# Performance work log

Hardware: AMD Instinct MI355X
Metric: run time of the kernel (lower is better)

The kernel has to match this reference:

```python
import jax, jax.numpy as jnp
import numpy as np

B, S, D, H, V = 4, 1024, 1024, 16, 1024
HD = D // H  # head_dim = 64
FF = 4 * D


def _layer_norm(x, g, b, eps=1e-5):
    mu = jnp.mean(x, axis=-1, keepdims=True)
    var = jnp.var(x, axis=-1, keepdims=True)
    return (x - mu) * jax.lax.rsqrt(var + eps) * g + b


def _pos_encoding(seq_len, d_model):
    # sinusoidal PE, matching PositionalEncoding buffer construction
    pos = jnp.arange(seq_len, dtype=jnp.float32)[:, None]
    div = jnp.exp(jnp.arange(0, d_model, 2, dtype=jnp.float32) * (-np.log(10000.0) / d_model))
    pe = jnp.zeros((seq_len, d_model), dtype=jnp.float32)
    pe = pe.at[:, 0::2].set(jnp.sin(pos * div))
    pe = pe.at[:, 1::2].set(jnp.cos(pos * div))
    return pe


def setup_inputs() -> dict:
    key = jax.random.key(0)
    ks = jax.random.split(key, 12)
    sc = 0.02
    return {
        "inputs": jax.random.randint(ks[0], (B, S), 0, V, dtype=jnp.int32),
        "targets": jax.random.randint(ks[1], (B, S), 0, V, dtype=jnp.int32),
        "wte": jax.random.normal(ks[2], (V, D), jnp.float32) * sc,
        "wq": jax.random.normal(ks[3], (D, D), jnp.float32) * sc,
        "bq": jnp.zeros((D,), jnp.float32),
        "wk": jax.random.normal(ks[4], (D, D), jnp.float32) * sc,
        "bk": jnp.zeros((D,), jnp.float32),
        "wv": jax.random.normal(ks[5], (D, D), jnp.float32) * sc,
        "bv": jnp.zeros((D,), jnp.float32),
        "wo": jax.random.normal(ks[6], (D, D), jnp.float32) * sc,
        "bo": jnp.zeros((D,), jnp.float32),
        "w1": jax.random.normal(ks[7], (D, FF), jnp.float32) * sc,
        "b1": jnp.zeros((FF,), jnp.float32),
        "w2": jax.random.normal(ks[8], (FF, D), jnp.float32) * sc,
        "b2": jnp.zeros((D,), jnp.float32),
        "ln1_g": jnp.ones((D,), jnp.float32),
        "ln1_b": jnp.zeros((D,), jnp.float32),
        "ln2_g": jnp.ones((D,), jnp.float32),
        "ln2_b": jnp.zeros((D,), jnp.float32),
    }


def reference(inputs, targets, wte, wq, bq, wk, bk, wv, bv, wo, bo,
              w1, b1, w2, b2, ln1_g, ln1_b, ln2_g, ln2_b):
    # embedding + positional encoding
    x = wte[inputs] + _pos_encoding(S, D)  # [B,S,D]

    # naive causal multi-head attention (dropout = identity in eval)
    q = (x @ wq + bq).reshape(B, S, H, HD)
    k = (x @ wk + bk).reshape(B, S, H, HD)
    v = (x @ wv + bv).reshape(B, S, H, HD)
    scores = jnp.einsum('bqhd,bkhd->bhqk', q, k) / np.sqrt(HD)  # [B,H,S,S]
    causal = jnp.tril(jnp.ones((S, S), dtype=bool))
    scores = jnp.where(causal, scores, -jnp.inf)
    attn = jax.nn.softmax(scores, axis=-1)
    ctx = jnp.einsum('bhqk,bkhd->bqhd', attn, v).reshape(B, S, D)
    att_out = ctx @ wo + bo

    # residual + LN1, FFN + GELU, residual + LN2
    adn = _layer_norm(x + att_out, ln1_g, ln1_b)
    h = jax.nn.gelu(adn @ w1 + b1, approximate=False) @ w2 + b2
    logits = _layer_norm(h + adn, ln2_g, ln2_b)

    # cross-entropy over d_model(=vocab) classes
    logits_flat = logits.reshape(B * S, D)
    tgt = targets.reshape(B * S)
    logp = jax.nn.log_softmax(logits_flat, axis=-1)
    loss = -jnp.mean(jnp.take_along_axis(logp, tgt[:, None], axis=-1))
    return logits_flat, loss
```

## Files before the change

### kernel.cpp

```cpp
#include <hip/hip_runtime.h>
#include <math.h>

#define BB 4
#define SS 1024
#define DD 1024
#define HH 16
#define HDIM 64
#define FF 4096
#define MM 4096

typedef short bf16x8 __attribute__((ext_vector_type(8)));
typedef short bf16x4 __attribute__((ext_vector_type(4)));
typedef float f32x4  __attribute__((ext_vector_type(4)));

static __device__ __forceinline__ short f2bf(float f){
  unsigned u = __float_as_uint(f);
  u += 0x7FFFu + ((u >> 16) & 1u);
  return (short)(u >> 16);
}
static __device__ __forceinline__ float b2f(short s){
  return __uint_as_float(((unsigned)(unsigned short)s) << 16);
}

static __device__ __forceinline__ float erf_fast(float x){
  float ax = fabsf(x);
  float t  = __builtin_amdgcn_rcpf(1.0f + 0.3275911f * ax);
  float p  = t * (0.254829592f + t * (-0.284496736f + t * (1.421413741f +
             t * (-1.453152027f + t * 1.061405429f))));
  float e  = 1.0f - p * __expf(-ax * ax);
  return copysignf(e, x);
}

static __device__ __forceinline__ void gl_lds16(const short* g, short* l){
  __builtin_amdgcn_global_load_lds((const __attribute__((address_space(1))) unsigned int*)g,
                                   (__attribute__((address_space(3))) unsigned int*)l,
                                   16, 0, 0);
}

#define MFMA_BF16 __builtin_amdgcn_mfma_f32_16x16x32_bf16

__global__ __launch_bounds__(256) void trans_all_kernel(
    const float* __restrict__ wq, const float* __restrict__ wk,
    const float* __restrict__ wv, const float* __restrict__ wo,
    const float* __restrict__ w1, const float* __restrict__ w2,
    short* __restrict__ wqkvt, short* __restrict__ wot,
    short* __restrict__ w1t,   short* __restrict__ w2t){
  __shared__ float t[32][33];
  int idx = blockIdx.x;
  const float* src; short* dst; int R, C, cx, ry;
  if (idx < 4096){
    int wsel = idx >> 10, tt = idx & 1023;
    cx = tt & 31; ry = tt >> 5; R = 1024; C = 1024;
    src = (wsel == 0) ? wq : (wsel == 1) ? wk : (wsel == 2) ? wv : wo;
    dst = (wsel == 3) ? wot : wqkvt + (size_t)wsel * 1024 * 1024;
  } else if (idx < 8192){
    int tt = idx - 4096; cx = tt & 127; ry = tt >> 7; R = 1024; C = 4096;
    src = w1; dst = w1t;
  } else {
    int tt = idx - 8192; cx = tt & 31; ry = tt >> 5; R = 4096; C = 1024;
    src = w2; dst = w2t;
  }
  int c0 = cx * 32, r0 = ry * 32;
  int tx = threadIdx.x, ty = threadIdx.y;
#pragma unroll
  for (int i = 0; i < 32; i += 8)
    t[ty + i][tx] = src[(size_t)(r0 + ty + i) * C + (c0 + tx)];
  __syncthreads();
#pragma unroll
  for (int i = 0; i < 32; i += 8)
    dst[(size_t)(c0 + ty + i) * R + (r0 + tx)] = f2bf(t[tx][ty + i]);
}

__global__ __launch_bounds__(256) void concat_bias_kernel(const float* __restrict__ a,
                                                          const float* __restrict__ b,
                                                          const float* __restrict__ c,
                                                          float* __restrict__ dst){
  int t = blockIdx.x * 256 + threadIdx.x;
  float v = (t < 1024) ? a[t] : (t < 2048 ? b[t - 1024] : c[t - 2048]);
  dst[t] = v;
}

__global__ __launch_bounds__(256) void embed_kernel(const int* __restrict__ inputs,
                                                    const float* __restrict__ wte,
                                                    short* __restrict__ xb){
  int idx4 = blockIdx.x * 256 + threadIdx.x;
  int row = idx4 >> 8;
  int d   = (idx4 & 255) * 4;
  int s   = row & (SS - 1);
  int tok = inputs[row];
  float4 w = *(const float4*)&wte[(size_t)tok * DD + d];
  const float cdiv = -9.210340371976184f / 512.0f;
  int i0 = d >> 1;
  float ang0 = (float)s * expf((float)i0 * cdiv);
  float ang1 = (float)s * expf((float)(i0 + 1) * cdiv);
  float x0 = w.x + sinf(ang0);
  float x1 = w.y + cosf(ang0);
  float x2 = w.z + sinf(ang1);
  float x3 = w.w + cosf(ang1);
  bf16x4 sb; sb[0]=f2bf(x0); sb[1]=f2bf(x1); sb[2]=f2bf(x2); sb[3]=f2bf(x3);
  *(bf16x4*)&xb[(size_t)row * DD + d] = sb;
}

template<int MODE, bool GELU, bool ADDBIAS>
__global__ __launch_bounds__(512, 2) void gemm256_kernel(const short* __restrict__ A,
    const short* __restrict__ Bt, const float* __restrict__ bias,
    short* __restrict__ o0, short* __restrict__ o1,
    short* __restrict__ o2, short* __restrict__ o3,
    short* __restrict__ qo, short* __restrict__ ko, short* __restrict__ vto,
    int M, int N, int K, int Kc){
  __shared__ __align__(16) short lds[8 * 8192];
  int tid = threadIdx.x;
  int lid = blockIdx.y * gridDim.x + blockIdx.x;
  int cpx = (gridDim.x * gridDim.y) >> 3;
  int swz = (lid & 7) * cpx + (lid >> 3);
  int n0 = (swz % gridDim.x) * 256;
  int m0 = (swz / gridDim.x) * 256;
  int bz = blockIdx.z;
  int kbeg = bz * Kc;
  int w = tid >> 6, lane = tid & 63, lr = lane & 15, lg = lane >> 4;
  int wm = w >> 2, wn = w & 3;
  f32x4 acc[8][4] = {};

  int sr = lane >> 3;
  int sg = (lane & 7) ^ sr;
  auto STAGE_HALF = [&](int buf, int typ, int half, int kt){
    const short* s0 = (typ ? Bt : A) + (size_t)kbeg + sg * 8;
    int rb = (typ ? n0 : m0) + half * 128 + w * 8 + sr;
#pragma unroll
    for (int j = 0; j < 2; j++)
      gl_lds16(s0 + (size_t)(rb + j * 64) * K + kt * 64,
               &lds[(((buf << 2) | (typ << 1) | half) << 13) + (j << 12) + (w << 9)]);
  };

  int nt = Kc >> 6;
  STAGE_HALF(0, 0, 0, 0); STAGE_HALF(0, 0, 1, 0);
  STAGE_HALF(0, 1, 0, 0); STAGE_HALF(0, 1, 1, 0);
  STAGE_HALF(1, 0, 0, 1); STAGE_HALF(1, 0, 1, 1);
  STAGE_HALF(1, 1, 0, 1); STAGE_HALF(1, 1, 1, 1);
  asm volatile("s_waitcnt vmcnt(8)" ::: "memory");
  __builtin_amdgcn_s_barrier();

  int lr64 = lr * 64;
  int ck0 = ((lg     ) ^ (lr & 7)) * 8;
  int ck1 = ((lg + 4 ) ^ (lr & 7)) * 8;
  int brow = (wn & 1) << 12;

  bf16x8 Alo[4][2], Ahi[4][2], Blo[2][2], Bhi[2][2];

#define ABASE(b) ((((b) << 2) | wm) << 13) + lr64
#define BBASE(b) ((((b) << 2) | 2 | (wn >> 1)) << 13) + brow + lr64
#define RD_ALO(b) { int ab_ = ABASE(b); _Pragma("unroll") for (int fi_ = 0; fi_ < 4; fi_++){ \
    Alo[fi_][0] = *(const bf16x8*)&lds[ab_ + fi_ * 1024 + ck0]; \
    Alo[fi_][1] = *(const bf16x8*)&lds[ab_ + fi_ * 1024 + ck1]; } }
#define RD_AHI(b) { int ab_ = ABASE(b); _Pragma("unroll") for (int fi_ = 0; fi_ < 4; fi_++){ \
    Ahi[fi_][0] = *(const bf16x8*)&lds[ab_ + (fi_ + 4) * 1024 + ck0]; \
    Ahi[fi_][1] = *(const bf16x8*)&lds[ab_ + (fi_ + 4) * 1024 + ck1]; } }
#define RD_BLO(b) { int bb_ = BBASE(b); _Pragma("unroll") for (int ni_ = 0; ni_ < 2; ni_++){ \
    Blo[ni_][0] = *(const bf16x8*)&lds[bb_ + ni_ * 1024 + ck0]; \
    Blo[ni_][1] = *(const bf16x8*)&lds[bb_ + ni_ * 1024 + ck1]; } }
#define RD_BHI(b) { int bb_ = BBASE(b); _Pragma("unroll") for (int ni_ = 0; ni_ < 2; ni_++){ \
    Bhi[ni_][0] = *(const bf16x8*)&lds[bb_ + (ni_ + 2) * 1024 + ck0]; \
    Bhi[ni_][1] = *(const bf16x8*)&lds[bb_ + (ni_ + 2) * 1024 + ck1]; } }
#define QUAD(MB, NB, AF, BF) \
    __builtin_amdgcn_s_setprio(1); \
    _Pragma("unroll") for (int mi_ = 0; mi_ < 4; mi_++) \
      _Pragma("unroll") for (int ni_ = 0; ni_ < 2; ni_++){ \
        acc[mi_ + MB][ni_ + NB] = MFMA_BF16(AF[mi_][0], BF[ni_][0], acc[mi_ + MB][ni_ + NB], 0, 0, 0); \
        acc[mi_ + MB][ni_ + NB] = MFMA_BF16(AF[mi_][1], BF[ni_][1], acc[mi_ + MB][ni_ + NB], 0, 0, 0); } \
    __builtin_amdgcn_s_setprio(0);

  RD_ALO(0); RD_BLO(0);

  for (int t = 0; t < nt; t++){
    int b = t & 1, bn = b ^ 1;
    RD_AHI(b);
    asm volatile("s_waitcnt lgkmcnt(8)" ::: "memory");
    __builtin_amdgcn_sched_barrier(0);
    QUAD(0, 0, Alo, Blo);
    __builtin_amdgcn_s_barrier();
    RD_BHI(b);
    if (t + 2 < nt){ STAGE_HALF(b, 0, 0, t + 2); STAGE_HALF(b, 0, 1, t + 2); }
    asm volatile("s_waitcnt lgkmcnt(4)" ::: "memory");
    __builtin_amdgcn_sched_barrier(0);
    QUAD(4, 0, Ahi, Blo);
    __builtin_amdgcn_s_barrier();
    if (t + 2 < nt) asm volatile("s_waitcnt vmcnt(4)" ::: "memory");
    else            asm volatile("s_waitcnt vmcnt(0)" ::: "memory");
    if (t + 2 < nt){ STAGE_HALF(b, 1, 0, t + 2); STAGE_HALF(b, 1, 1, t + 2); }
    asm volatile("s_waitcnt lgkmcnt(0)" ::: "memory");
    __builtin_amdgcn_sched_barrier(0);
    QUAD(4, 2, Ahi, Bhi);
    __builtin_amdgcn_s_barrier();
    QUAD(0, 2, Alo, Bhi);
    __builtin_amdgcn_sched_barrier(0);
    if (t + 1 < nt){ RD_ALO(bn); RD_BLO(bn); }
    __builtin_amdgcn_s_barrier();
  }
#undef QUAD
#undef RD_BHI
#undef RD_BLO
#undef RD_AHI
#undef RD_ALO
#undef BBASE
#undef ABASE

  short* slab = (MODE == 1) ? ((bz == 0) ? o0 : (bz == 1) ? o1 : (bz == 2) ? o2 : o3) : o0;
  bool addb = ADDBIAS && (MODE != 1 || bz == 0);
#pragma unroll
  for (int mi = 0; mi < 8; mi++){
#pragma unroll
    for (int ni = 0; ni < 4; ni++){
      int ng = n0 + wn * 64 + ni * 16 + lr;
      float bv = addb ? bias[ng] : 0.0f;
      int mg0 = m0 + wm * 128 + mi * 16 + 4 * lg;
      if (MODE == 2){
        int sel = n0 >> 10;
        if (sel == 2){
          int d = ng & 1023; int hh = d >> 6, nn = d & 63;
          int bI = mg0 >> 10, sI = mg0 & 1023;
          bf16x4 pk;
#pragma unroll
          for (int r = 0; r < 4; r++) pk[r] = f2bf(acc[mi][ni][r] + bv);
          *(bf16x4*)&vto[(((size_t)(bI * HH + hh)) * HDIM + nn) * SS + sI] = pk;
        } else {
          short* dst = (sel == 0) ? qo : ko;
          float qscl = (sel == 0) ? 0.125f : 1.0f;
#pragma unroll
          for (int r = 0; r < 4; r++)
            dst[(size_t)(mg0 + r) * DD + (ng & 1023)] = f2bf((acc[mi][ni][r] + bv) * qscl);
        }
      } else {
#pragma unroll
        for (int r = 0; r < 4; r++){
          float v = acc[mi][ni][r] + bv;
          if (GELU) v = 0.5f * v * (1.0f + erf_fast(v * 0.70710678118654752f));
          slab[(size_t)(mg0 + r) * N + ng] = f2bf(v);
        }
      }
    }
  }
}

__global__ __launch_bounds__(256) void attn_kernel(const short* __restrict__ qb,
                                                   const short* __restrict__ kb,
                                                   const short* __restrict__ vtb,
                                                   short* __restrict__ ctxb){
  __shared__ __align__(16) short k_lds[2][64 * 64];
  __shared__ __align__(16) short v_lds[2][64 * 64];
  __shared__ __align__(16) short p_lds[4][2][16 * 72];
  int qp = blockIdx.x, h = blockIdx.y, b = blockIdx.z;
  int Tlo = qp, Thi = 15 - qp;
  int tid = threadIdx.x, w = tid >> 6, lane = tid & 63, lr = lane & 15, lg = lane >> 4;

  const short* kp0 = kb  + (size_t)b * SS * DD + h * HDIM;
  const short* vt0 = vtb + (size_t)(b * HH + h) * HDIM * SS;

  bf16x8 qf0[2], qf1[2];
#pragma unroll
  for (int ti = 0; ti < 2; ti++){
    int T = ti ? Thi : Tlo;
    const short* qp_ = qb + ((size_t)(b * SS + T * 64 + w * 16 + lr) * DD + h * HDIM);
    qf0[ti] = *(const bf16x8*)&qp_[lg * 8];
    qf1[ti] = *(const bf16x8*)&qp_[32 + lg * 8];
  }

  bf16x8 ones;
#pragma unroll
  for (int j = 0; j < 8; j++) ones[j] = (short)0x3F80;

  float m[2][4], l[2][4];
  f32x4 acc[2][4] = {};
#pragma unroll
  for (int ti = 0; ti < 2; ti++)
#pragma unroll
    for (int r = 0; r < 4; r++){ m[ti][r] = -1e30f; l[ti][r] = 0.0f; }

  int srow8 = lane >> 3;
  int sjs   = (lane & 7) ^ srow8;
  auto STAGE = [&](int buf, int kt){
#pragma unroll
    for (int i = 0; i < 2; i++){
      int rb  = (w + 4 * i) * 8;
      int row = rb + srow8;
      gl_lds16(kp0 + (size_t)(kt * 64 + row) * DD + sjs * 8, &k_lds[buf][rb * 64]);
      gl_lds16(vt0 + (size_t)row * SS + kt * 64 + sjs * 8,   &v_lds[buf][rb * 64]);
    }
  };

  int cur = 0;
  STAGE(0, 0);
  asm volatile("s_waitcnt vmcnt(0)" ::: "memory");
  __syncthreads();

  bf16x8 pf0[2], pf1[2];
  for (int kt = 0; kt <= Thi; kt++){
    if (kt < Thi) STAGE(cur ^ 1, kt + 1);

    bf16x8 kf0[4], kf1[4];
#pragma unroll
    for (int sub = 0; sub < 4; sub++){
      int r = sub * 16 + lr;
      kf0[sub] = *(const bf16x8*)&k_lds[cur][r * 64 + ((lg     ^ (r & 7)) * 8)];
      kf1[sub] = *(const bf16x8*)&k_lds[cur][r * 64 + (((lg+4) ^ (r & 7)) * 8)];
    }

#pragma unroll
    for (int ti = 0; ti < 2; ti++){
      int T = ti ? Thi : Tlo;
      if (kt > T) continue;
      f32x4 sc4[4];
      __builtin_amdgcn_s_setprio(1);
#pragma unroll
      for (int sub = 0; sub < 4; sub++){
        f32x4 t = {};
        t = MFMA_BF16(qf0[ti], kf0[sub], t, 0, 0, 0);
        t = MFMA_BF16(qf1[ti], kf1[sub], t, 0, 0, 0);
        sc4[sub] = t;
      }
      __builtin_amdgcn_s_setprio(0);
      if (kt == T){
#pragma unroll
        for (int sub = 0; sub < 4; sub++)
#pragma unroll
          for (int r = 0; r < 4; r++)
            if (16 * sub + lr > 16 * w + 4 * lg + r) sc4[sub][r] = -1e30f;
      }

      float pm[4];
#pragma unroll
      for (int r = 0; r < 4; r++)
        pm[r] = fmaxf(fmaxf(sc4[0][r], sc4[1][r]), fmaxf(sc4[2][r], sc4[3][r]));
#pragma unroll
      for (int off = 1; off < 16; off <<= 1)
#pragma unroll
        for (int r = 0; r < 4; r++) pm[r] = fmaxf(pm[r], __shfl_xor(pm[r], off));

      float dmax = fmaxf(fmaxf(pm[0] - m[ti][0], pm[1] - m[ti][1]),
                         fmaxf(pm[2] - m[ti][2], pm[3] - m[ti][3]));
      if (!__all(dmax <= 8.0f)){
        float scl[4];
#pragma unroll
        for (int r = 0; r < 4; r++){
          float mn = fmaxf(m[ti][r], pm[r]);
          scl[r] = __expf(m[ti][r] - mn);
          m[ti][r] = mn;
          l[ti][r] *= scl[r];
        }
#pragma unroll
        for (int nb = 0; nb < 4; nb++)
#pragma unroll
          for (int r = 0; r < 4; r++) acc[ti][nb][r] *= scl[r];
      }

      short* pw = &p_lds[w][ti][0];
#pragma unroll
      for (int sub = 0; sub < 4; sub++)
#pragma unroll
        for (int r = 0; r < 4; r++)
          pw[(4 * lg + r) * 72 + sub * 16 + lr] = f2bf(__expf(sc4[sub][r] - m[ti][r]));
      pf0[ti] = *(const bf16x8*)&pw[lr * 72 + lg * 8];
      pf1[ti] = *(const bf16x8*)&pw[lr * 72 + 32 + lg * 8];
    }

    bf16x8 vf0[4], vf1[4];
#pragma unroll
    for (int nb = 0; nb < 4; nb++){
      int r = nb * 16 + lr;
      vf0[nb] = *(const bf16x8*)&v_lds[cur][r * 64 + ((lg     ^ (r & 7)) * 8)];
      vf1[nb] = *(const bf16x8*)&v_lds[cur][r * 64 + (((lg+4) ^ (r & 7)) * 8)];
    }

#pragma unroll
    for (int ti = 0; ti < 2; ti++){
      int T = ti ? Thi : Tlo;
      if (kt > T) continue;
      f32x4 rsum = {};
      __builtin_amdgcn_s_setprio(1);
      rsum = MFMA_BF16(pf0[ti], ones, rsum, 0, 0, 0);
      rsum = MFMA_BF16(pf1[ti], ones, rsum, 0, 0, 0);
#pragma unroll
      for (int nb = 0; nb < 4; nb++){
        acc[ti][nb] = MFMA_BF16(pf0[ti], vf0[nb], acc[ti][nb], 0, 0, 0);
        acc[ti][nb] = MFMA_BF16(pf1[ti], vf1[nb], acc[ti][nb], 0, 0, 0);
      }
      __builtin_amdgcn_s_setprio(0);
#pragma unroll
      for (int r = 0; r < 4; r++) l[ti][r] += rsum[r];
    }

    asm volatile("s_waitcnt vmcnt(0)" ::: "memory");
    __syncthreads();
    cur ^= 1;
  }

#pragma unroll
  for (int ti = 0; ti < 2; ti++){
    int T = ti ? Thi : Tlo;
#pragma unroll
    for (int r = 0; r < 4; r++){
      float inv = 1.0f / l[ti][r];
      int row = T * 64 + w * 16 + 4 * lg + r;
#pragma unroll
      for (int nb = 0; nb < 4; nb++)
        ctxb[(size_t)(b * SS + row) * DD + h * HDIM + nb * 16 + lr] = f2bf(acc[ti][nb][r] * inv);
    }
  }
}

template<int NPART, bool WF32, bool LOSS>
__global__ __launch_bounds__(256) void ln_kernel(const short* __restrict__ p0,
                                                 const short* __restrict__ p1,
                                                 const short* __restrict__ p2,
                                                 const short* __restrict__ p3,
                                                 const short* __restrict__ resb,
                                                 const float* __restrict__ g,
                                                 const float* __restrict__ be,
                                                 float* __restrict__ of,
                                                 short* __restrict__ ob,
                                                 const int* __restrict__ tgt,
                                                 float* __restrict__ lrow){
  int row = blockIdx.x, tid = threadIdx.x;
  size_t base = (size_t)row * DD + tid * 4;
  bf16x4 rv = *(const bf16x4*)&resb[base];
  float x0 = b2f(rv[0]), x1 = b2f(rv[1]), x2 = b2f(rv[2]), x3 = b2f(rv[3]);
  const short* ps[4] = {p0, p1, p2, p3};
#pragma unroll
  for (int p = 0; p < NPART; p++){
    bf16x4 pv = *(const bf16x4*)&ps[p][base];
    x0 += b2f(pv[0]); x1 += b2f(pv[1]); x2 += b2f(pv[2]); x3 += b2f(pv[3]);
  }
  float s = x0 + x1 + x2 + x3;
  float q = x0 * x0 + x1 * x1 + x2 * x2 + x3 * x3;
#pragma unroll
  for (int off = 32; off; off >>= 1){ s += __shfl_xor(s, off); q += __shfl_xor(q, off); }
  __shared__ float red[9];
  if ((tid & 63) == 0){ red[tid >> 6] = s; red[4 + (tid >> 6)] = q; }
  __syncthreads();
  s = red[0] + red[1] + red[2] + red[3];
  q = red[4] + red[5] + red[6] + red[7];
  float mean = s * (1.0f / DD);
  float var  = q * (1.0f / DD) - mean * mean;
  float rstd = rsqrtf(var + 1e-5f);
  float4 gv  = *(const float4*)&g[tid * 4];
  float4 bev = *(const float4*)&be[tid * 4];
  float y0 = (x0 - mean) * rstd * gv.x + bev.x;
  float y1 = (x1 - mean) * rstd * gv.y + bev.y;
  float y2 = (x2 - mean) * rstd * gv.z + bev.z;
  float y3 = (x3 - mean) * rstd * gv.w + bev.w;
  if (WF32){
    *(float4*)&of[base] = make_float4(y0, y1, y2, y3);
  } else {
    bf16x4 sb; sb[0]=f2bf(y0); sb[1]=f2bf(y1); sb[2]=f2bf(y2); sb[3]=f2bf(y3);
    *(bf16x4*)&ob[base] = sb;
  }
  if (LOSS){
    __syncthreads();
    float mx = fmaxf(fmaxf(y0, y1), fmaxf(y2, y3));
#pragma unroll
    for (int off = 32; off; off >>= 1) mx = fmaxf(mx, __shfl_xor(mx, off));
    if ((tid & 63) == 0) red[tid >> 6] = mx;
    int t = tgt[row];
    if (tid == (t >> 2))
      red[8] = ((t & 3) == 0) ? y0 : ((t & 3) == 1) ? y1 : ((t & 3) == 2) ? y2 : y3;
    __syncthreads();
    mx = fmaxf(fmaxf(red[0], red[1]), fmaxf(red[2], red[3]));
    float se = __expf(y0 - mx) + __expf(y1 - mx) + __expf(y2 - mx) + __expf(y3 - mx);
#pragma unroll
    for (int off = 32; off; off >>= 1) se += __shfl_xor(se, off);
    if ((tid & 63) == 0) red[4 + (tid >> 6)] = se;
    __syncthreads();
    if (tid == 0){
      float tot = red[4] + red[5] + red[6] + red[7];
      lrow[row] = mx + logf(tot) - red[8];
    }
  }
}

__global__ __launch_bounds__(256) void loss_reduce_kernel(const float* __restrict__ pr,
                                                          float* __restrict__ outp){
  int tid = threadIdx.x;
  float s = 0.0f;
  for (int i = tid; i < MM; i += 256) s += pr[i];
#pragma unroll
  for (int off = 32; off; off >>= 1) s += __shfl_xor(s, off);
  __shared__ float red[4];
  if ((tid & 63) == 0) red[tid >> 6] = s;
  __syncthreads();
  if (tid == 0) outp[0] = (red[0] + red[1] + red[2] + red[3]) * (1.0f / MM);
}

extern "C" void kernel_launch(void* const* d_in, const int* in_sizes, int n_in,
                              void* d_out, int out_size, void* d_ws, size_t ws_size,
                              hipStream_t stream){
  const int*   inputs  = (const int*)  d_in[0];
  const int*   targets = (const int*)  d_in[1];
  const float* wte     = (const float*)d_in[2];
  const float* wq      = (const float*)d_in[3];
  const float* bq      = (const float*)d_in[4];
  const float* wk      = (const float*)d_in[5];
  const float* bk      = (const float*)d_in[6];
  const float* wv      = (const float*)d_in[7];
  const float* bvv     = (const float*)d_in[8];
  const float* wo      = (const float*)d_in[9];
  const float* bo      = (const float*)d_in[10];
  const float* w1      = (const float*)d_in[11];
  const float* b1      = (const float*)d_in[12];
  const float* w2      = (const float*)d_in[13];
  const float* b2      = (const float*)d_in[14];
  const float* ln1g    = (const float*)d_in[15];
  const float* ln1b    = (const float*)d_in[16];
  const float* ln2g    = (const float*)d_in[17];
  const float* ln2b    = (const float*)d_in[18];
  float* out = (float*)d_out;

  char* ws = (char*)d_ws;
  const size_t MB = 1024 * 1024;
  short* wqkvt = (short*)(ws + 0 * MB);
  short* wot   = (short*)(ws + 6 * MB);
  short* w1t   = (short*)(ws + 8 * MB);
  short* w2t   = (short*)(ws + 16 * MB);
  short* xb    = (short*)(ws + 24 * MB);
  short* qbuf  = (short*)(ws + 32 * MB);
  short* kbuf  = (short*)(ws + 40 * MB);
  short* vtb   = (short*)(ws + 48 * MB);
  short* ctxb  = (short*)(ws + 56 * MB);
  short* pr0   = (short*)(ws + 64 * MB);
  short* pr1   = (short*)(ws + 72 * MB);
  short* pr2   = (short*)(ws + 80 * MB);
  short* pr3   = (short*)(ws + 88 * MB);
  short* adnb  = (short*)(ws + 96 * MB);
  short* h1b   = (short*)(ws + 32 * MB);
  short* hs0   = (short*)(ws + 64 * MB);
  short* hs1   = (short*)(ws + 72 * MB);
  short* hs2   = (short*)(ws + 80 * MB);
  short* hs3   = (short*)(ws + 88 * MB);
  float* lrow  = (float*)(ws + 104 * MB);
  float* bqkv  = (float*)(ws + 105 * MB);

  trans_all_kernel<<<12288, dim3(32, 8), 0, stream>>>(
      wq, wk, wv, wo, w1, w2, wqkvt, wot, w1t, w2t);
  concat_bias_kernel<<<12, 256, 0, stream>>>(bq, bk, bvv, bqkv);

  embed_kernel<<<4096, 256, 0, stream>>>(inputs, wte, xb);

  gemm256_kernel<2, false, true><<<dim3(12, 16), 512, 0, stream>>>(
      xb, wqkvt, bqkv, nullptr, nullptr, nullptr, nullptr,
      qbuf, kbuf, vtb, MM, 3 * DD, DD, DD);

  attn_kernel<<<dim3(8, 16, 4), 256, 0, stream>>>(qbuf, kbuf, vtb, ctxb);

  gemm256_kernel<1, false, true><<<dim3(4, 16, 4), 512, 0, stream>>>(
      ctxb, wot, bo, pr0, pr1, pr2, pr3,
      nullptr, nullptr, nullptr, MM, DD, DD, 256);

  ln_kernel<4, false, false><<<4096, 256, 0, stream>>>(
      pr0, pr1, pr2, pr3, xb, ln1g, ln1b, nullptr, adnb, nullptr, nullptr);

  gemm256_kernel<0, true, true><<<dim3(16, 16), 512, 0, stream>>>(
      adnb, w1t, b1, h1b, nullptr, nullptr, nullptr,
      nullptr, nullptr, nullptr, MM, FF, DD, DD);

  gemm256_kernel<1, false, true><<<dim3(4, 16, 4), 512, 0, stream>>>(
      h1b, w2t, b2, hs0, hs1, hs2, hs3,
      nullptr, nullptr, nullptr, MM, DD, FF, 1024);

  ln_kernel<4, true, true><<<4096, 256, 0, stream>>>(
      hs0, hs1, hs2, hs3, adnb, ln2g, ln2b, out, nullptr, targets, lrow);

  loss_reduce_kernel<<<1, 256, 0, stream>>>(lrow, out + (size_t)MM * DD);
}
```

Before: 219.2 us.

## Add 128x256-tile GEMM variant for output projection and FFN GEMMs

Introduces a new GEMM kernel that uses a 128x256 output tile instead of 256x256, with 8 waves laid out 2x4 and each wave computing 64x64. It double-buffers LDS, uses XOR-swizzled LDS reads, and applies a block-id swizzle for L2 locality. The output projection, FFN1 and FFN2 GEMMs switch to it with twice as many blocks, aiming for better CU occupancy and load balance on the 256-CU device. The cost is lower arithmetic intensity per block and more redundant B-tile loads.

```diff
diff --git a/kernel.cpp b/kernel.cpp
--- a/kernel.cpp
+++ b/kernel.cpp
@@ -241,6 +241,90 @@
   }
 }
 
+template<int MODE, bool GELU, bool ADDBIAS>
+__global__ __launch_bounds__(512) void gemmw_kernel(const short* __restrict__ A,
+    const short* __restrict__ Bt, const float* __restrict__ bias,
+    short* __restrict__ o0, short* __restrict__ o1,
+    short* __restrict__ o2, short* __restrict__ o3,
+    int M, int N, int K, int Kc){
+  __shared__ __align__(16) short lds[2][12288];
+  int tid = threadIdx.x;
+  int lid = blockIdx.y * gridDim.x + blockIdx.x;
+  int cpx = (gridDim.x * gridDim.y) >> 3;
+  int swz = (lid & 7) * cpx + (lid >> 3);
+  int n0 = (swz % gridDim.x) * 256;
+  int m0 = (swz / gridDim.x) * 128;
+  int bz = blockIdx.z;
+  int kbeg = bz * Kc;
+  int w = tid >> 6, lane = tid & 63, lr = lane & 15, lg = lane >> 4;
+  int wm = w >> 2, wn = w & 3;
+  f32x4 acc[4][4] = {};
+
+  int sr = lane >> 2;
+  int sg = (lane & 3) ^ ((lane >> 3) & 3);
+  const short* Arow = A  + (size_t)(m0 + w * 16 + sr) * K + kbeg + sg * 8;
+  const short* Brow = Bt + (size_t)(n0 + w * 16 + sr) * K + kbeg + sg * 8;
+
+  auto STAGE = [&](int buf, int kt){
+    int k0 = kt * 32;
+    gl_lds16(Arow + k0, &lds[buf][w * 512]);
+#pragma unroll
+    for (int j = 0; j < 2; j++)
+      gl_lds16(Brow + (size_t)(j * 128) * K + k0, &lds[buf][4096 + j * 4096 + w * 512]);
+  };
+
+  int nst = Kc >> 5;
+  STAGE(0, 0);
+  asm volatile("s_waitcnt vmcnt(0)" ::: "memory");
+  __builtin_amdgcn_s_barrier();
+
+  int cxor = ((lr >> 1) & 3) * 8;
+
+  for (int it = 0; it < nst; it++){
+    int cur = it & 1;
+    if (it + 1 < nst) STAGE(cur ^ 1, it + 1);
+
+    bf16x8 af[4], bfr[4];
+#pragma unroll
+    for (int mi = 0; mi < 4; mi++){
+      int row = wm * 64 + mi * 16 + lr;
+      af[mi] = *(const bf16x8*)&lds[cur][row * 32 + ((lg * 8) ^ cxor)];
+    }
+#pragma unroll
+    for (int ni = 0; ni < 4; ni++){
+      int row = wn * 64 + ni * 16 + lr;
+      bfr[ni] = *(const bf16x8*)&lds[cur][4096 + row * 32 + ((lg * 8) ^ cxor)];
+    }
+    __builtin_amdgcn_s_setprio(1);
+#pragma unroll
+    for (int mi = 0; mi < 4; mi++)
+#pragma unroll
+      for (int ni = 0; ni < 4; ni++)
+        acc[mi][ni] = MFMA_BF16(af[mi], bfr[ni], acc[mi][ni], 0, 0, 0);
+    __builtin_amdgcn_s_setprio(0);
+    asm volatile("s_waitcnt vmcnt(0) lgkmcnt(0)" ::: "memory");
+    __builtin_amdgcn_s_barrier();
+  }
+
+  short* slab = (MODE == 1) ? ((bz == 0) ? o0 : (bz == 1) ? o1 : (bz == 2) ? o2 : o3) : o0;
+  bool addb = ADDBIAS && (MODE != 1 || bz == 0);
+#pragma unroll
+  for (int mi = 0; mi < 4; mi++){
+#pragma unroll
+    for (int ni = 0; ni < 4; ni++){
+      int ng = n0 + wn * 64 + ni * 16 + lr;
+      float bv = addb ? bias[ng] : 0.0f;
+      int mg0 = m0 + wm * 64 + mi * 16 + 4 * lg;
+#pragma unroll
+      for (int r = 0; r < 4; r++){
+        float v = acc[mi][ni][r] + bv;
+        if (GELU) v = 0.5f * v * (1.0f + erf_fast(v * 0.70710678118654752f));
+        slab[(size_t)(mg0 + r) * N + ng] = f2bf(v);
+      }
+    }
+  }
+}
+
 __global__ __launch_bounds__(256) void attn_kernel(const short* __restrict__ qb,
                                                    const short* __restrict__ kb,
                                                    const short* __restrict__ vtb,
@@ -549,20 +633,17 @@
 
   attn_kernel<<<dim3(8, 16, 4), 256, 0, stream>>>(qbuf, kbuf, vtb, ctxb);
 
-  gemm256_kernel<1, false, true><<<dim3(4, 16, 4), 512, 0, stream>>>(
-      ctxb, wot, bo, pr0, pr1, pr2, pr3,
-      nullptr, nullptr, nullptr, MM, DD, DD, 256);
+  gemmw_kernel<1, false, true><<<dim3(4, 32, 4), 512, 0, stream>>>(
+      ctxb, wot, bo, pr0, pr1, pr2, pr3, MM, DD, DD, 256);
 
   ln_kernel<4, false, false><<<4096, 256, 0, stream>>>(
       pr0, pr1, pr2, pr3, xb, ln1g, ln1b, nullptr, adnb, nullptr, nullptr);
 
-  gemm256_kernel<0, true, true><<<dim3(16, 16), 512, 0, stream>>>(
-      adnb, w1t, b1, h1b, nullptr, nullptr, nullptr,
-      nullptr, nullptr, nullptr, MM, FF, DD, DD);
-
-  gemm256_kernel<1, false, true><<<dim3(4, 16, 4), 512, 0, stream>>>(
-      h1b, w2t, b2, hs0, hs1, hs2, hs3,
-      nullptr, nullptr, nullptr, MM, DD, FF, 1024);
+  gemmw_kernel<0, true, true><<<dim3(16, 32), 512, 0, stream>>>(
+      adnb, w1t, b1, h1b, nullptr, nullptr, nullptr, MM, FF, DD, DD);
+
+  gemmw_kernel<1, false, true><<<dim3(4, 32, 4), 512, 0, stream>>>(
+      h1b, w2t, b2, hs0, hs1, hs2, hs3, MM, DD, FF, 1024);
 
   ln_kernel<4, true, true><<<4096, 256, 0, stream>>>(
       hs0, hs1, hs2, hs3, adnb, ln2g, ln2b, out, nullptr, targets, lrow);
```

After: 220.0 us. Within noise of the previous version (+0.3%).
